# Kernel optimization log

Hardware: AMD Instinct MI355X
Metric: run time of the kernel (lower is better)

## Reference

```python
import jax, jax.numpy as jnp
import numpy as np

H = 16
D = 64
EPS = 1e-6

def _phi(x):
    # elu_feature_map: elu(x) + 1
    return jax.nn.elu(x) + 1.0

def setup_inputs() -> dict:
    key = jax.random.key(0)
    k1, k2, k3, k4 = jax.random.split(key, 4)
    B, N = 4, 4096
    query = jax.random.normal(k1, (B, N, H * D), dtype=jnp.float32)
    key_t = jax.random.normal(k2, (B, N, H * D), dtype=jnp.float32)
    value = jax.random.normal(k3, (B, N, H * D), dtype=jnp.float32)
    W_out = jax.random.normal(k4, (D, H * D), dtype=jnp.float32) * (1.0 / np.sqrt(H * D))
    b_out = jnp.zeros((D,), dtype=jnp.float32)
    return {"query": query, "key": key_t, "value": value, "W_out": W_out, "b_out": b_out}

def reference(query, key, value, W_out, b_out):
    B, N, _ = query.shape
    # b n (h d) -> b h n d
    def split_heads(x):
        return x.reshape(B, N, H, D).transpose(0, 2, 1, 3)
    q = split_heads(query)
    k = split_heads(key)
    v = split_heads(value)
    Q = _phi(q)  # [B,H,N,D]
    K = _phi(k)
    # KV aggregation: O(N D^2)
    KV = jnp.einsum('bhnd,bhnm->bhdm', K, v)          # [B,H,D,D]
    Ksum = K.sum(axis=2)                               # [B,H,D]
    Z = 1.0 / (jnp.einsum('bhnd,bhd->bhn', Q, Ksum) + EPS)  # [B,H,N]
    out = jnp.einsum('bhnd,bhdm,bhn->bhnm', Q, KV, Z)  # [B,H,N,D]
    # b h n d -> b n h d -> (b*n, h*d)
    out = out.transpose(0, 2, 1, 3).reshape(B * N, H * D)
    return out @ W_out.T + b_out
```

## Files before the change

kernel.cpp:

```cpp
#include <hip/hip_runtime.h>

#define B_  4
#define N_  4096
#define H_  16
#define BH_ 64
#define S_  16
#define HS_ 4
#define ST_ 72
#define EPS_ 1e-6f

typedef _Float16 h2  __attribute__((ext_vector_type(2)));
typedef _Float16 h8  __attribute__((ext_vector_type(8)));
typedef float    f4v __attribute__((ext_vector_type(4)));

struct H2x2 { h2 a, b; };
struct H2x4 { h2 e[4]; };

__device__ __forceinline__ h8 ld_h8(const _Float16* p) {
    f4v r = *(const f4v*)p;
    return __builtin_bit_cast(h8, r);
}
__device__ __forceinline__ H2x4 ld_h2x4(const _Float16* p) {
    f4v r = *(const f4v*)p;
    return __builtin_bit_cast(H2x4, r);
}
__device__ __forceinline__ void st_h2x2(_Float16* p, h2 a, h2 b) {
    H2x2 t{a, b};
    *(float2*)p = __builtin_bit_cast(float2, t);
}
__device__ __forceinline__ float phi(float x) {
    return x > 0.0f ? x + 1.0f : __expf(x);
}
__device__ __forceinline__ float fdot2(h2 a, h2 b, float c) {
    return __builtin_amdgcn_fdot2(a, b, c, false);
}
__device__ __forceinline__ void barrier_lgkm() {
    asm volatile("s_waitcnt lgkmcnt(0)" ::: "memory");
    __builtin_amdgcn_sched_barrier(0);
    __builtin_amdgcn_s_barrier();
}

__global__ __launch_bounds__(256, 4) void k_kvpart(const float* __restrict__ K,
                                                   const float* __restrict__ V,
                                                   float* __restrict__ kvpart,
                                                   float* __restrict__ kspart) {
    const int bh = blockIdx.x, s = blockIdx.y;
    const int b = bh >> 4, h = bh & 15;
    const int t = threadIdx.x, w = t >> 6, lane = t & 63;
    const int rp = t >> 4, c4 = t & 15;

    __shared__ __align__(16) _Float16 pool[2 * 2 * 64 * ST_];
    __shared__ float ksred[4][64];

    const f4v* Kf4 = (const f4v*)K;
    const f4v* Vf4 = (const f4v*)V;

    f4v kA[4], vA[4], kB[4], vB[4];

    auto LOADX = [&](f4v* kreg, f4v* vreg, int chunk) {
        const int n0 = s * (N_ / S_) + chunk * 64;
        size_t g = (size_t)(b * N_ + n0 + 4 * rp) * 256 + h * 16 + c4;
        kreg[0] = Kf4[g];       kreg[1] = Kf4[g + 256];
        kreg[2] = Kf4[g + 512]; kreg[3] = Kf4[g + 768];
        vreg[0] = Vf4[g];       vreg[1] = Vf4[g + 256];
        vreg[2] = Vf4[g + 512]; vreg[3] = Vf4[g + 768];
    };
    auto STOREX = [&](const f4v* kreg, const f4v* vreg, int buf) {
        _Float16* Kt = pool + buf * (2 * 64 * ST_);
        _Float16* Vt = Kt + 64 * ST_;
#pragma unroll
        for (int dj = 0; dj < 4; ++dj) {
            int d = 4 * c4 + dj;
            h2 lo, hi;
            lo.x = (_Float16)phi(kreg[0][dj]); lo.y = (_Float16)phi(kreg[1][dj]);
            hi.x = (_Float16)phi(kreg[2][dj]); hi.y = (_Float16)phi(kreg[3][dj]);
            st_h2x2(&Kt[d * ST_ + 4 * rp], lo, hi);
            lo.x = (_Float16)vreg[0][dj]; lo.y = (_Float16)vreg[1][dj];
            hi.x = (_Float16)vreg[2][dj]; hi.y = (_Float16)vreg[3][dj];
            st_h2x2(&Vt[d * ST_ + 4 * rp], lo, hi);
        }
    };

    const int td0 = 2 * (w >> 1);
    const int tj0 = 2 * (w & 1);
    const int rA  = lane & 15;
    const int fo  = (lane >> 4) * 8;

    f4v acc[2][2];
#pragma unroll
    for (int a = 0; a < 2; ++a)
#pragma unroll
        for (int bb = 0; bb < 2; ++bb) acc[a][bb] = (f4v){0.f, 0.f, 0.f, 0.f};
    float ksum_acc = 0.f;
    h2 one2; one2.x = (_Float16)1.0f; one2.y = (_Float16)1.0f;

    auto COMPUTE = [&](int buf) {
        const _Float16* Kt = pool + buf * (2 * 64 * ST_);
        const _Float16* Vt = Kt + 64 * ST_;
#pragma unroll
        for (int ks = 0; ks < 2; ++ks) {
            h8 a0 = ld_h8(&Kt[(16 * (td0 + 0) + rA) * ST_ + ks * 32 + fo]);
            h8 a1 = ld_h8(&Kt[(16 * (td0 + 1) + rA) * ST_ + ks * 32 + fo]);
            h8 b0 = ld_h8(&Vt[(16 * (tj0 + 0) + rA) * ST_ + ks * 32 + fo]);
            h8 b1 = ld_h8(&Vt[(16 * (tj0 + 1) + rA) * ST_ + ks * 32 + fo]);
            acc[0][0] = __builtin_amdgcn_mfma_f32_16x16x32_f16(a0, b0, acc[0][0], 0, 0, 0);
            acc[0][1] = __builtin_amdgcn_mfma_f32_16x16x32_f16(a0, b1, acc[0][1], 0, 0, 0);
            acc[1][0] = __builtin_amdgcn_mfma_f32_16x16x32_f16(a1, b0, acc[1][0], 0, 0, 0);
            acc[1][1] = __builtin_amdgcn_mfma_f32_16x16x32_f16(a1, b1, acc[1][1], 0, 0, 0);
        }
        {
            int d = t & 63, qtr = t >> 6;
            H2x4 x0 = ld_h2x4(&Kt[d * ST_ + qtr * 16]);
            H2x4 x1 = ld_h2x4(&Kt[d * ST_ + qtr * 16 + 8]);
#pragma unroll
            for (int i = 0; i < 4; ++i) {
                ksum_acc = fdot2(x0.e[i], one2, ksum_acc);
                ksum_acc = fdot2(x1.e[i], one2, ksum_acc);
            }
        }
    };

    LOADX(kA, vA, 0);
    LOADX(kB, vB, 1);
    STOREX(kA, vA, 0);
    barrier_lgkm();
    LOADX(kA, vA, 2);
    COMPUTE(0);
    STOREX(kB, vB, 1);
    barrier_lgkm();
    LOADX(kB, vB, 3);
    COMPUTE(1);
    STOREX(kA, vA, 0);
    barrier_lgkm();
    COMPUTE(0);
    STOREX(kB, vB, 1);
    barrier_lgkm();
    COMPUTE(1);

    float* outp = kvpart + (size_t)(bh * S_ + s) * 4096;
#pragma unroll
    for (int a = 0; a < 2; ++a)
#pragma unroll
        for (int bb = 0; bb < 2; ++bb)
#pragma unroll
            for (int r = 0; r < 4; ++r) {
                int d = 16 * (td0 + a) + (lane >> 4) * 4 + r;
                int m = 16 * (tj0 + bb) + (lane & 15);
                outp[d * 64 + m] = acc[a][bb][r];
            }
    ksred[t >> 6][t & 63] = ksum_acc;
    __syncthreads();
    if (t < 64) {
        kspart[(size_t)(bh * S_ + s) * 64 + t] =
            ksred[0][t] + ksred[1][t] + ksred[2][t] + ksred[3][t];
    }
}

__global__ __launch_bounds__(256, 4) void k_makeM(const float* __restrict__ kvpart,
                                                  const float* __restrict__ kspart,
                                                  const float* __restrict__ W,
                                                  _Float16* __restrict__ Mt,
                                                  float* __restrict__ Ksum) {
    const int bh = blockIdx.x, dq = blockIdx.y;
    const int h  = bh & 15;
    const int t  = threadIdx.x;

    __shared__ float KVs[16][68];
    __shared__ float Ws[64][68];

    const f4v* kv4 = (const f4v*)kvpart;
    const f4v* W4  = (const f4v*)W;

    {
        int row = t >> 4, c4 = t & 15;
        f4v rr[S_];
#pragma unroll
        for (int s = 0; s < S_; ++s)
            rr[s] = kv4[(size_t)(bh * S_ + s) * 1024 + (dq * 16 + row) * 16 + c4];
        f4v r = {0.f, 0.f, 0.f, 0.f};
#pragma unroll
        for (int s = 0; s < S_; ++s) r += rr[s];
        *(f4v*)&KVs[row][c4 * 4] = r;
    }
    for (int idx = t; idx < 1024; idx += 256) {
        int wrow = idx >> 4, wc = idx & 15;
        *(f4v*)&Ws[wrow][wc * 4] = W4[(size_t)wrow * 256 + h * 16 + wc];
    }
    if (dq == 0 && t < 64) {
        float ksl[S_];
#pragma unroll
        for (int s = 0; s < S_; ++s) ksl[s] = kspart[(size_t)(bh * S_ + s) * 64 + t];
        float ks = 0.f;
#pragma unroll
        for (int s = 0; s < S_; ++s) ks += ksl[s];
        Ksum[(size_t)bh * 64 + t] = ks;
    }
    __syncthreads();

    const int j = t >> 2, dl = (t & 3) * 4;
    float acc[4] = {0.f, 0.f, 0.f, 0.f};
#pragma unroll 4
    for (int m4 = 0; m4 < 16; ++m4) {
        f4v wr  = *(const f4v*)&Ws[j][m4 * 4];
        f4v kv0 = *(const f4v*)&KVs[dl + 0][m4 * 4];
        f4v kv1 = *(const f4v*)&KVs[dl + 1][m4 * 4];
        f4v kv2 = *(const f4v*)&KVs[dl + 2][m4 * 4];
        f4v kv3 = *(const f4v*)&KVs[dl + 3][m4 * 4];
        acc[0] += wr[0] * kv0[0] + wr[1] * kv0[1] + wr[2] * kv0[2] + wr[3] * kv0[3];
        acc[1] += wr[0] * kv1[0] + wr[1] * kv1[1] + wr[2] * kv1[2] + wr[3] * kv1[3];
        acc[2] += wr[0] * kv2[0] + wr[1] * kv2[1] + wr[2] * kv2[2] + wr[3] * kv2[3];
        acc[3] += wr[0] * kv3[0] + wr[1] * kv3[1] + wr[2] * kv3[2] + wr[3] * kv3[3];
    }
    h2 lo, hi;
    lo.x = (_Float16)acc[0]; lo.y = (_Float16)acc[1];
    hi.x = (_Float16)acc[2]; hi.y = (_Float16)acc[3];
    H2x2 pk{lo, hi};
    *(float2*)&Mt[((size_t)bh * 64 + j) * 64 + dq * 16 + dl] =
        __builtin_bit_cast(float2, pk);
}

__global__ __launch_bounds__(256, 4) void k_out(const float* __restrict__ Q,
                                                const _Float16* __restrict__ Mtg,
                                                const float* __restrict__ Ksum,
                                                float* __restrict__ outpart) {
    const int nc = blockIdx.x, b = blockIdx.y, hs = blockIdx.z;
    const int n0 = nc * 64;
    const int t = threadIdx.x, w = t >> 6, lane = t & 63;
    const int rp4 = t >> 4, c4 = t & 15;

    __shared__ __align__(16) _Float16 pool[2 * 2 * 64 * ST_];
    __shared__ float zz[64];
    __shared__ h2 Kss[2][32];

    const f4v* Qf4 = (const f4v*)Q;

    f4v qr[4], mr[2];
    float ksa = 0.f, ksb = 0.f;
    auto LOAD = [&](int hh) {
        const int h = hs * 4 + hh, bh = b * 16 + h;
        size_t g = (size_t)(b * N_ + n0 + rp4) * 256 + h * 16 + c4;
        qr[0] = Qf4[g];            qr[1] = Qf4[g + 16 * 256];
        qr[2] = Qf4[g + 32 * 256]; qr[3] = Qf4[g + 48 * 256];
        mr[0] = ((const f4v*)Mtg)[(size_t)bh * 512 + t];
        mr[1] = ((const f4v*)Mtg)[(size_t)bh * 512 + t + 256];
        if (t < 32) {
            ksa = Ksum[(size_t)bh * 64 + 2 * t];
            ksb = Ksum[(size_t)bh * 64 + 2 * t + 1];
        }
    };
    auto STORE = [&](int buf) {
        _Float16* Qp = pool + buf * (2 * 64 * ST_);
        _Float16* Mt = Qp + 64 * ST_;
#pragma unroll
        for (int r = 0; r < 4; ++r) {
            int row = rp4 + 16 * r;
            h2 p0, p1;
            p0.x = (_Float16)phi(qr[r][0]); p0.y = (_Float16)phi(qr[r][1]);
            p1.x = (_Float16)phi(qr[r][2]); p1.y = (_Float16)phi(qr[r][3]);
            st_h2x2(&Qp[row * ST_ + 4 * c4], p0, p1);
        }
        *(f4v*)&Mt[(t >> 3) * ST_ + (t & 7) * 8] = mr[0];
        *(f4v*)&Mt[((t + 256) >> 3) * ST_ + (t & 7) * 8] = mr[1];
        if (t < 32) { h2 kk; kk.x = (_Float16)ksa; kk.y = (_Float16)ksb; Kss[buf][t] = kk; }
    };

    const int tn0 = 2 * (w >> 1), tj0 = 2 * (w & 1);
    const int rA = lane & 15, fo = (lane >> 4) * 8;
    float facc[2][2][4] = {{{0.f}}};

    LOAD(0);
    STORE(0);

    for (int hh = 0; hh < 4; ++hh) {
        if (hh + 1 < 4) LOAD(hh + 1);
        barrier_lgkm();
        const int buf = hh & 1;
        const _Float16* Qp = pool + buf * (2 * 64 * ST_);
        const _Float16* Mt = Qp + 64 * ST_;

        if (t < 64) {
            float zp = 0.f;
#pragma unroll
            for (int c = 0; c < 8; ++c) {
                H2x4 x = ld_h2x4(&Qp[t * ST_ + c * 8]);
#pragma unroll
                for (int i = 0; i < 4; ++i) zp = fdot2(x.e[i], Kss[buf][c * 4 + i], zp);
            }
            zz[t] = 1.0f / (zp + EPS_);
        }
        barrier_lgkm();

        f4v acc[2][2];
#pragma unroll
        for (int a = 0; a < 2; ++a)
#pragma unroll
            for (int bb = 0; bb < 2; ++bb) acc[a][bb] = (f4v){0.f, 0.f, 0.f, 0.f};
#pragma unroll
        for (int ks = 0; ks < 2; ++ks) {
            h8 a0 = ld_h8(&Qp[(16 * (tn0 + 0) + rA) * ST_ + ks * 32 + fo]);
            h8 a1 = ld_h8(&Qp[(16 * (tn0 + 1) + rA) * ST_ + ks * 32 + fo]);
            h8 b0 = ld_h8(&Mt[(16 * (tj0 + 0) + rA) * ST_ + ks * 32 + fo]);
            h8 b1 = ld_h8(&Mt[(16 * (tj0 + 1) + rA) * ST_ + ks * 32 + fo]);
            acc[0][0] = __builtin_amdgcn_mfma_f32_16x16x32_f16(a0, b0, acc[0][0], 0, 0, 0);
            acc[0][1] = __builtin_amdgcn_mfma_f32_16x16x32_f16(a0, b1, acc[0][1], 0, 0, 0);
            acc[1][0] = __builtin_amdgcn_mfma_f32_16x16x32_f16(a1, b0, acc[1][0], 0, 0, 0);
            acc[1][1] = __builtin_amdgcn_mfma_f32_16x16x32_f16(a1, b1, acc[1][1], 0, 0, 0);
        }
#pragma unroll
        for (int a = 0; a < 2; ++a)
#pragma unroll
            for (int r = 0; r < 4; ++r) {
                int row = 16 * (tn0 + a) + (lane >> 4) * 4 + r;
                float z = zz[row];
                facc[a][0][r] += z * acc[a][0][r];
                facc[a][1][r] += z * acc[a][1][r];
            }
        if (hh + 1 < 4) STORE((hh + 1) & 1);
    }

    float* op = outpart + (size_t)hs * (B_ * N_ * 64);
#pragma unroll
    for (int a = 0; a < 2; ++a)
#pragma unroll
        for (int bb = 0; bb < 2; ++bb)
#pragma unroll
            for (int r = 0; r < 4; ++r) {
                int n = 16 * (tn0 + a) + (lane >> 4) * 4 + r;
                int j = 16 * (tj0 + bb) + (lane & 15);
                op[(size_t)(b * N_ + n0 + n) * 64 + j] = facc[a][bb][r];
            }
}

__global__ __launch_bounds__(256, 4) void k_red(const float* __restrict__ outpart,
                                                const float* __restrict__ bout,
                                                float* __restrict__ out) {
    const int p = blockIdx.x * 256 + threadIdx.x;
    const f4v* P4 = (const f4v*)outpart;
    const f4v* B4 = (const f4v*)bout;
    f4v o = B4[p & 15];
    const int stride = B_ * N_ * 64 / 4;
    f4v pr[HS_];
#pragma unroll
    for (int hs = 0; hs < HS_; ++hs) pr[hs] = P4[(size_t)hs * stride + p];
#pragma unroll
    for (int hs = 0; hs < HS_; ++hs) o += pr[hs];
    ((f4v*)out)[p] = o;
}

extern "C" void kernel_launch(void* const* d_in, const int* in_sizes, int n_in,
                              void* d_out, int out_size, void* d_ws, size_t ws_size,
                              hipStream_t stream) {
    const float* q  = (const float*)d_in[0];
    const float* k  = (const float*)d_in[1];
    const float* v  = (const float*)d_in[2];
    const float* W  = (const float*)d_in[3];
    const float* bo = (const float*)d_in[4];
    float* out = (float*)d_out;

    float* ws      = (float*)d_ws;
    float* kvpart  = ws;
    float* kspart  = kvpart + (size_t)BH_ * S_ * 4096;
    float* Mt      = kspart + (size_t)BH_ * S_ * 64;
    float* Ksum    = Mt + (size_t)BH_ * 4096 / 2;
    float* outpart = Ksum + (size_t)BH_ * 64;

    k_kvpart<<<dim3(BH_, S_), 256, 0, stream>>>(k, v, kvpart, kspart);
    k_makeM<<<dim3(BH_, 4), 256, 0, stream>>>(kvpart, kspart, W, (_Float16*)Mt, Ksum);
    k_out<<<dim3(N_ / 64, B_, HS_), 256, 0, stream>>>(q, (const _Float16*)Mt, Ksum, outpart);
    k_red<<<B_ * N_ * 64 / 4 / 256, 256, 0, stream>>>(outpart, bo, out);
}
```

Before: 225.0 us.

## Restructure KV partial kernel to process four heads per block with coalesced loads

```diff
diff --git a/kernel.cpp b/kernel.cpp
--- a/kernel.cpp
+++ b/kernel.cpp
@@ -9,6 +9,10 @@
 #define ST_ 72
 #define EPS_ 1e-6f
 
+#define NST_ 40
+#define TSH_ 2584
+#define BUFH_ (8 * TSH_)
+
 typedef _Float16 h2  __attribute__((ext_vector_type(2)));
 typedef _Float16 h8  __attribute__((ext_vector_type(8)));
 typedef float    f4v __attribute__((ext_vector_type(4)));
@@ -40,17 +44,16 @@
     __builtin_amdgcn_s_barrier();
 }
 
-__global__ __launch_bounds__(256, 4) void k_kvpart(const float* __restrict__ K,
+__global__ __launch_bounds__(512, 2) void k_kvpart(const float* __restrict__ K,
                                                    const float* __restrict__ V,
                                                    float* __restrict__ kvpart,
                                                    float* __restrict__ kspart) {
-    const int bh = blockIdx.x, s = blockIdx.y;
-    const int b = bh >> 4, h = bh & 15;
-    const int t = threadIdx.x, w = t >> 6, lane = t & 63;
-    const int rp = t >> 4, c4 = t & 15;
-
-    __shared__ __align__(16) _Float16 pool[2 * 2 * 64 * ST_];
-    __shared__ float ksred[4][64];
+    const int s = blockIdx.x, hq = blockIdx.y, b = blockIdx.z;
+    const int t = threadIdx.x, wv = t >> 6, lane = t & 63;
+    const int hp = lane >> 4;
+    const int l15 = lane & 15;
+
+    __shared__ __align__(16) _Float16 pool[2 * BUFH_];
 
     const f4v* Kf4 = (const f4v*)K;
     const f4v* Vf4 = (const f4v*)V;
@@ -58,101 +61,101 @@
     f4v kA[4], vA[4], kB[4], vB[4];
 
     auto LOADX = [&](f4v* kreg, f4v* vreg, int chunk) {
-        const int n0 = s * (N_ / S_) + chunk * 64;
-        size_t g = (size_t)(b * N_ + n0 + 4 * rp) * 256 + h * 16 + c4;
+        const int n0 = s * 256 + chunk * 32 + 4 * wv;
+        size_t g = (size_t)(b * N_ + n0) * 256 + hq * 64 + lane;
         kreg[0] = Kf4[g];       kreg[1] = Kf4[g + 256];
         kreg[2] = Kf4[g + 512]; kreg[3] = Kf4[g + 768];
         vreg[0] = Vf4[g];       vreg[1] = Vf4[g + 256];
         vreg[2] = Vf4[g + 512]; vreg[3] = Vf4[g + 768];
     };
     auto STOREX = [&](const f4v* kreg, const f4v* vreg, int buf) {
-        _Float16* Kt = pool + buf * (2 * 64 * ST_);
-        _Float16* Vt = Kt + 64 * ST_;
+        _Float16* Kt = pool + buf * BUFH_ + (hp * 2) * TSH_;
+        _Float16* Vt = Kt + TSH_;
+        const int nn = 4 * wv;
 #pragma unroll
         for (int dj = 0; dj < 4; ++dj) {
-            int d = 4 * c4 + dj;
+            int d = 4 * l15 + dj;
             h2 lo, hi;
             lo.x = (_Float16)phi(kreg[0][dj]); lo.y = (_Float16)phi(kreg[1][dj]);
             hi.x = (_Float16)phi(kreg[2][dj]); hi.y = (_Float16)phi(kreg[3][dj]);
-            st_h2x2(&Kt[d * ST_ + 4 * rp], lo, hi);
+            st_h2x2(&Kt[d * NST_ + nn], lo, hi);
             lo.x = (_Float16)vreg[0][dj]; lo.y = (_Float16)vreg[1][dj];
             hi.x = (_Float16)vreg[2][dj]; hi.y = (_Float16)vreg[3][dj];
-            st_h2x2(&Vt[d * ST_ + 4 * rp], lo, hi);
-        }
-    };
-
-    const int td0 = 2 * (w >> 1);
-    const int tj0 = 2 * (w & 1);
-    const int rA  = lane & 15;
-    const int fo  = (lane >> 4) * 8;
-
-    f4v acc[2][2];
+            st_h2x2(&Vt[d * NST_ + nn], lo, hi);
+        }
+    };
+
+    const int hh = wv >> 1, dhalf = wv & 1;
+    const int rA = l15;
+    const int fo = (lane >> 4) * 8;
+
+    f4v acc[2][4];
 #pragma unroll
     for (int a = 0; a < 2; ++a)
 #pragma unroll
-        for (int bb = 0; bb < 2; ++bb) acc[a][bb] = (f4v){0.f, 0.f, 0.f, 0.f};
-    float ksum_acc = 0.f;
-    h2 one2; one2.x = (_Float16)1.0f; one2.y = (_Float16)1.0f;
+        for (int m = 0; m < 4; ++m) acc[a][m] = (f4v){0.f, 0.f, 0.f, 0.f};
+    f4v accK[2];
+    accK[0] = (f4v){0.f, 0.f, 0.f, 0.f};
+    accK[1] = (f4v){0.f, 0.f, 0.f, 0.f};
+    h8 ones;
+#pragma unroll
+    for (int i = 0; i < 8; ++i) ones[i] = (_Float16)1.0f;
 
     auto COMPUTE = [&](int buf) {
-        const _Float16* Kt = pool + buf * (2 * 64 * ST_);
-        const _Float16* Vt = Kt + 64 * ST_;
-#pragma unroll
-        for (int ks = 0; ks < 2; ++ks) {
-            h8 a0 = ld_h8(&Kt[(16 * (td0 + 0) + rA) * ST_ + ks * 32 + fo]);
-            h8 a1 = ld_h8(&Kt[(16 * (td0 + 1) + rA) * ST_ + ks * 32 + fo]);
-            h8 b0 = ld_h8(&Vt[(16 * (tj0 + 0) + rA) * ST_ + ks * 32 + fo]);
-            h8 b1 = ld_h8(&Vt[(16 * (tj0 + 1) + rA) * ST_ + ks * 32 + fo]);
-            acc[0][0] = __builtin_amdgcn_mfma_f32_16x16x32_f16(a0, b0, acc[0][0], 0, 0, 0);
-            acc[0][1] = __builtin_amdgcn_mfma_f32_16x16x32_f16(a0, b1, acc[0][1], 0, 0, 0);
-            acc[1][0] = __builtin_amdgcn_mfma_f32_16x16x32_f16(a1, b0, acc[1][0], 0, 0, 0);
-            acc[1][1] = __builtin_amdgcn_mfma_f32_16x16x32_f16(a1, b1, acc[1][1], 0, 0, 0);
-        }
-        {
-            int d = t & 63, qtr = t >> 6;
-            H2x4 x0 = ld_h2x4(&Kt[d * ST_ + qtr * 16]);
-            H2x4 x1 = ld_h2x4(&Kt[d * ST_ + qtr * 16 + 8]);
-#pragma unroll
-            for (int i = 0; i < 4; ++i) {
-                ksum_acc = fdot2(x0.e[i], one2, ksum_acc);
-                ksum_acc = fdot2(x1.e[i], one2, ksum_acc);
-            }
-        }
+        const _Float16* Kt = pool + buf * BUFH_ + (hh * 2) * TSH_;
+        const _Float16* Vt = Kt + TSH_;
+        h8 a0 = ld_h8(&Kt[(32 * dhalf + rA) * NST_ + fo]);
+        h8 a1 = ld_h8(&Kt[(32 * dhalf + 16 + rA) * NST_ + fo]);
+        h8 b0 = ld_h8(&Vt[(rA) * NST_ + fo]);
+        h8 b1 = ld_h8(&Vt[(16 + rA) * NST_ + fo]);
+        h8 b2 = ld_h8(&Vt[(32 + rA) * NST_ + fo]);
+        h8 b3 = ld_h8(&Vt[(48 + rA) * NST_ + fo]);
+        acc[0][0] = __builtin_amdgcn_mfma_f32_16x16x32_f16(a0, b0, acc[0][0], 0, 0, 0);
+        acc[0][1] = __builtin_amdgcn_mfma_f32_16x16x32_f16(a0, b1, acc[0][1], 0, 0, 0);
+        acc[0][2] = __builtin_amdgcn_mfma_f32_16x16x32_f16(a0, b2, acc[0][2], 0, 0, 0);
+        acc[0][3] = __builtin_amdgcn_mfma_f32_16x16x32_f16(a0, b3, acc[0][3], 0, 0, 0);
+        acc[1][0] = __builtin_amdgcn_mfma_f32_16x16x32_f16(a1, b0, acc[1][0], 0, 0, 0);
+        acc[1][1] = __builtin_amdgcn_mfma_f32_16x16x32_f16(a1, b1, acc[1][1], 0, 0, 0);
+        acc[1][2] = __builtin_amdgcn_mfma_f32_16x16x32_f16(a1, b2, acc[1][2], 0, 0, 0);
+        acc[1][3] = __builtin_amdgcn_mfma_f32_16x16x32_f16(a1, b3, acc[1][3], 0, 0, 0);
+        accK[0]   = __builtin_amdgcn_mfma_f32_16x16x32_f16(a0, ones, accK[0], 0, 0, 0);
+        accK[1]   = __builtin_amdgcn_mfma_f32_16x16x32_f16(a1, ones, accK[1], 0, 0, 0);
     };
 
     LOADX(kA, vA, 0);
     LOADX(kB, vB, 1);
     STOREX(kA, vA, 0);
     barrier_lgkm();
-    LOADX(kA, vA, 2);
-    COMPUTE(0);
-    STOREX(kB, vB, 1);
-    barrier_lgkm();
-    LOADX(kB, vB, 3);
+    LOADX(kA, vA, 2); COMPUTE(0); STOREX(kB, vB, 1); barrier_lgkm();
+    LOADX(kB, vB, 3); COMPUTE(1); STOREX(kA, vA, 0); barrier_lgkm();
+    LOADX(kA, vA, 4); COMPUTE(0); STOREX(kB, vB, 1); barrier_lgkm();
+    LOADX(kB, vB, 5); COMPUTE(1); STOREX(kA, vA, 0); barrier_lgkm();
+    LOADX(kA, vA, 6); COMPUTE(0); STOREX(kB, vB, 1); barrier_lgkm();
+    LOADX(kB, vB, 7); COMPUTE(1); STOREX(kA, vA, 0); barrier_lgkm();
+    COMPUTE(0); STOREX(kB, vB, 1); barrier_lgkm();
     COMPUTE(1);
-    STOREX(kA, vA, 0);
-    barrier_lgkm();
-    COMPUTE(0);
-    STOREX(kB, vB, 1);
-    barrier_lgkm();
-    COMPUTE(1);
-
+
+    const int bh = b * 16 + hq * 4 + hh;
     float* outp = kvpart + (size_t)(bh * S_ + s) * 4096;
 #pragma unroll
     for (int a = 0; a < 2; ++a)
 #pragma unroll
-        for (int bb = 0; bb < 2; ++bb)
+        for (int m = 0; m < 4; ++m)
 #pragma unroll
             for (int r = 0; r < 4; ++r) {
-                int d = 16 * (td0 + a) + (lane >> 4) * 4 + r;
-                int m = 16 * (tj0 + bb) + (lane & 15);
-                outp[d * 64 + m] = acc[a][bb][r];
-            }
-    ksred[t >> 6][t & 63] = ksum_acc;
-    __syncthreads();
-    if (t < 64) {
-        kspart[(size_t)(bh * S_ + s) * 64 + t] =
-            ksred[0][t] + ksred[1][t] + ksred[2][t] + ksred[3][t];
+                int d = 32 * dhalf + 16 * a + hp * 4 + r;
+                int mm = 16 * m + l15;
+                outp[d * 64 + mm] = acc[a][m][r];
+            }
+    if (l15 == 0) {
+        float* ksp = kspart + (size_t)(bh * S_ + s) * 64;
+#pragma unroll
+        for (int a = 0; a < 2; ++a)
+#pragma unroll
+            for (int r = 0; r < 4; ++r) {
+                int d = 32 * dhalf + 16 * a + hp * 4 + r;
+                ksp[d] = accK[a][r];
+            }
     }
 }
 
@@ -364,7 +367,7 @@
     float* Ksum    = Mt + (size_t)BH_ * 4096 / 2;
     float* outpart = Ksum + (size_t)BH_ * 64;
 
-    k_kvpart<<<dim3(BH_, S_), 256, 0, stream>>>(k, v, kvpart, kspart);
+    k_kvpart<<<dim3(S_, 4, 4), 512, 0, stream>>>(k, v, kvpart, kspart);
     k_makeM<<<dim3(BH_, 4), 256, 0, stream>>>(kvpart, kspart, W, (_Float16*)Mt, Ksum);
     k_out<<<dim3(N_ / 64, B_, HS_), 256, 0, stream>>>(q, (const _Float16*)Mt, Ksum, outpart);
     k_red<<<B_ * N_ * 64 / 4 / 256, 256, 0, stream>>>(outpart, bo, out);
```

New measurement: 222.0 us. About the same (-1.3%).
